# Kernel optimization log

Hardware: AMD Instinct MI355X
Metric: run time of the kernel (lower is better)

Reference implementation:

```python
import jax, jax.numpy as jnp
import numpy as np

B, P, M, C = 64, 8732, 16, 81
THRESHOLD = 0.5
NEG_POS_RATIO = 3
ALPHA = 1.0  # config.reg_weights
EPS = 1e-7


def cxcy_to_xy(c):
    return jnp.concatenate([c[..., :2] - c[..., 2:] / 2.0,
                            c[..., :2] + c[..., 2:] / 2.0], axis=-1)


def _rand_boxes_cxcy(key, shape):
    k1, k2 = jax.random.split(key)
    cxcy = jax.random.uniform(k1, shape + (2,), minval=0.2, maxval=0.8)
    wh = jax.random.uniform(k2, shape + (2,), minval=0.05, maxval=0.35)
    return jnp.concatenate([cxcy, wh], axis=-1)


def setup_inputs() -> dict:
    key = jax.random.key(0)
    ks = jax.random.split(key, 5)
    predicted_locs = cxcy_to_xy(_rand_boxes_cxcy(ks[0], (B, P)))          # valid corner boxes
    predicted_scores = jax.random.normal(ks[1], (B, P, C), dtype=jnp.float32)
    boxes = jnp.clip(cxcy_to_xy(_rand_boxes_cxcy(ks[2], (B, M))), 0.0, 1.0)  # GT corner boxes
    labels = jax.random.randint(ks[3], (B, M), 1, C)                       # object labels (1..C-1)
    priors_cxcy = _rand_boxes_cxcy(ks[4], (P,))
    return {"predicted_locs": predicted_locs, "predicted_scores": predicted_scores,
            "boxes": boxes, "labels": labels, "priors_cxcy": priors_cxcy}


def jaccard(a, b):
    # a: [M,4], b: [P,4] corner boxes -> [M,P] IoU
    lt = jnp.maximum(a[:, None, :2], b[None, :, :2])
    rb = jnp.minimum(a[:, None, 2:], b[None, :, 2:])
    wh = jnp.clip(rb - lt, 0.0)
    inter = wh[..., 0] * wh[..., 1]
    area_a = (a[:, 2] - a[:, 0]) * (a[:, 3] - a[:, 1])
    area_b = (b[:, 2] - b[:, 0]) * (b[:, 3] - b[:, 1])
    return inter / (area_a[:, None] + area_b[None, :] - inter)


def diou_loss(b1, b2):
    # corner boxes, elementwise over leading dims -> per-box loss 1 - DIoU
    lt = jnp.maximum(b1[..., :2], b2[..., :2])
    rb = jnp.minimum(b1[..., 2:], b2[..., 2:])
    wh = jnp.clip(rb - lt, 0.0)
    inter = wh[..., 0] * wh[..., 1]
    area1 = (b1[..., 2] - b1[..., 0]) * (b1[..., 3] - b1[..., 1])
    area2 = (b2[..., 2] - b2[..., 0]) * (b2[..., 3] - b2[..., 1])
    iou = inter / (area1 + area2 - inter + EPS)
    c1 = (b1[..., :2] + b1[..., 2:]) / 2.0
    c2 = (b2[..., :2] + b2[..., 2:]) / 2.0
    inter_diag = jnp.sum((c1 - c2) ** 2, axis=-1)
    enc_lt = jnp.minimum(b1[..., :2], b2[..., :2])
    enc_rb = jnp.maximum(b1[..., 2:], b2[..., 2:])
    outer_diag = jnp.sum((enc_rb - enc_lt) ** 2, axis=-1)
    dious = jnp.clip(iou - inter_diag / (outer_diag + EPS), -1.0, 1.0)
    return 1.0 - dious


def reference(predicted_locs, predicted_scores, boxes, labels, priors_cxcy):
    priors_xy = cxcy_to_xy(priors_cxcy)

    def assign(boxes_i, labels_i):
        overlap = jaccard(boxes_i, priors_xy)              # [M, P]
        ovl_prior = overlap.max(axis=0)                    # best overlap per prior
        obj_prior = overlap.argmax(axis=0)                 # best object per prior
        ovl_obj = overlap.max(axis=1)                      # best overlap per object
        prior_obj = overlap.argmax(axis=1)                 # best prior per object
        valid = ovl_obj > 0
        j_idx = jnp.cumsum(valid.astype(jnp.int32)) - 1    # index within filtered list (faithful)
        idx = jnp.where(valid, prior_obj, P)               # P -> dropped (out of bounds)
        ovl_prior = ovl_prior.at[idx].set(1.0, mode='drop')
        obj_prior = obj_prior.at[idx].set(j_idx, mode='drop')
        lab = labels_i[obj_prior]
        label_pos = jnp.where(ovl_prior < THRESHOLD, 0, lab)
        label_neg = jnp.where(ovl_prior < THRESHOLD - 0.1, -1, lab)
        return label_pos, label_neg

    true_classes, true_neg_classes = jax.vmap(assign)(boxes, labels)  # [B,P] each
    positive = true_classes > 0                                        # [B,P]
    pos_f = positive.astype(jnp.float32)
    n_pos_total = jnp.sum(pos_f)

    # Localization loss: DIoU(pred_pos, pred_pos) with reduce='mean' (faithful to source)
    per_box = diou_loss(predicted_locs, predicted_locs)                # [B,P]
    loc_loss = jnp.sum(per_box * pos_f) / jnp.maximum(n_pos_total, 1.0)

    # Confidence loss: per-prior CE + hard-negative mining (neg_pos_ratio)
    logp = jax.nn.log_softmax(predicted_scores, axis=-1)
    conf_all = -jnp.take_along_axis(logp, true_classes[..., None], axis=-1)[..., 0]  # [B,P]
    conf_pos_sum = jnp.sum(conf_all * pos_f)
    conf_neg = jnp.where(positive, 0.0, conf_all)
    conf_neg_sorted = -jnp.sort(-conf_neg, axis=-1)                    # descending
    n_hard = NEG_POS_RATIO * jnp.sum(positive, axis=1)                 # [B]
    hard_mask = (jnp.arange(P)[None, :] < n_hard[:, None]).astype(jnp.float32)
    conf_loss = (jnp.sum(conf_neg_sorted * hard_mask) + conf_pos_sum) / n_pos_total

    return conf_loss + ALPHA * loc_loss
```

## Files before the change

### kernel.cpp

```cpp
#include <hip/hip_runtime.h>
#include <math.h>

#define B_ 64
#define P_ 8732
#define M_ 16
#define C_ 81
#define THRESH 0.5f
#define EPS_ 1e-7f

#define CE_TILE 64
#define NBLK_CE ((B_ * P_) / CE_TILE)

__global__ __launch_bounds__(1024) void assign_kernel(
    const float* __restrict__ boxes,
    const int*   __restrict__ labels,
    const float* __restrict__ priors,
    int*         __restrict__ true_classes,
    int*         __restrict__ n_pos)
{
    const int b = blockIdx.x;
    const int tid = threadIdx.x;
    const int lane = tid & 63;
    const int wv = tid >> 6;

    __shared__ float s_ovl[P_];
    __shared__ unsigned char s_obj[P_];
    __shared__ float s_bx[M_][4];
    __shared__ float s_barea[M_];
    __shared__ int   s_lab[M_];
    __shared__ float s_wv[M_][16];
    __shared__ int   s_wp[M_][16];
    __shared__ float s_ovl_obj[M_];
    __shared__ int   s_prior_obj[M_];
    __shared__ int   s_cnt[16];

    if (tid < M_*4) ((float*)s_bx)[tid] = boxes[b*M_*4 + tid];
    if (tid < M_)   s_lab[tid] = labels[b*M_ + tid];
    __syncthreads();
    if (tid < M_)
        s_barea[tid] = (s_bx[tid][2]-s_bx[tid][0])*(s_bx[tid][3]-s_bx[tid][1]);
    __syncthreads();

    float bestv[M_]; int bestp[M_];
    #pragma unroll
    for (int m = 0; m < M_; ++m) { bestv[m] = -1.0f; bestp[m] = 0x7fffffff; }

    for (int p = tid; p < P_; p += 1024) {
        float4 pc = ((const float4*)priors)[p];
        float px1 = pc.x - pc.z*0.5f, py1 = pc.y - pc.w*0.5f;
        float px2 = pc.x + pc.z*0.5f, py2 = pc.y + pc.w*0.5f;
        float parea = (px2-px1)*(py2-py1);
        float bv = -1.0f; int bm = 0;
        #pragma unroll
        for (int m = 0; m < M_; ++m) {
            float ix1 = fmaxf(s_bx[m][0], px1);
            float iy1 = fmaxf(s_bx[m][1], py1);
            float ix2 = fminf(s_bx[m][2], px2);
            float iy2 = fminf(s_bx[m][3], py2);
            float iw = fmaxf(ix2-ix1, 0.0f);
            float ih = fmaxf(iy2-iy1, 0.0f);
            float inter = iw*ih;
            float iou = inter / (s_barea[m] + parea - inter);
            if (iou > bv) { bv = iou; bm = m; }
            if (iou > bestv[m]) { bestv[m] = iou; bestp[m] = p; }
        }
        s_ovl[p] = bv;
        s_obj[p] = (unsigned char)bm;
    }

    #pragma unroll
    for (int m = 0; m < M_; ++m) {
        float v = bestv[m]; int p = bestp[m];
        #pragma unroll
        for (int o = 32; o; o >>= 1) {
            float v2 = __shfl_xor(v, o);
            int   p2 = __shfl_xor(p, o);
            if (v2 > v || (v2 == v && p2 < p)) { v = v2; p = p2; }
        }
        if (lane == 0) { s_wv[m][wv] = v; s_wp[m][wv] = p; }
    }
    __syncthreads();

    if (tid < M_) {
        float v = s_wv[tid][0]; int p = s_wp[tid][0];
        #pragma unroll
        for (int w = 1; w < 16; ++w) {
            float v2 = s_wv[tid][w]; int p2 = s_wp[tid][w];
            if (v2 > v || (v2 == v && p2 < p)) { v = v2; p = p2; }
        }
        s_ovl_obj[tid] = v; s_prior_obj[tid] = p;
    }
    __syncthreads();

    if (tid == 0) {
        int cnt = 0;
        for (int m = 0; m < M_; ++m) {
            if (s_ovl_obj[m] > 0.0f) {
                int p = s_prior_obj[m];
                s_ovl[p] = 1.0f;
                s_obj[p] = (unsigned char)cnt;
                cnt++;
            }
        }
    }
    __syncthreads();

    int cpos = 0;
    for (int p = tid; p < P_; p += 1024) {
        int tc = 0;
        if (!(s_ovl[p] < THRESH)) tc = s_lab[s_obj[p]];
        true_classes[(size_t)b*P_ + p] = tc;
        cpos += (tc > 0);
    }
    #pragma unroll
    for (int o = 32; o; o >>= 1) cpos += __shfl_xor(cpos, o);
    if (lane == 0) s_cnt[wv] = cpos;
    __syncthreads();
    if (tid == 0) {
        int t = 0;
        #pragma unroll
        for (int w = 0; w < 16; ++w) t += s_cnt[w];
        n_pos[b] = t;
    }
}

__global__ __launch_bounds__(256) void ce_loc_kernel(
    const float* __restrict__ scores,
    const float* __restrict__ locs,
    const int*   __restrict__ tcls,
    float*       __restrict__ conf_neg,
    float*       __restrict__ blk_pos,
    float*       __restrict__ blk_loc)
{
    __shared__ float s[CE_TILE * C_];
    __shared__ int   s_tc[CE_TILE];
    __shared__ float s_cf[CE_TILE];
    __shared__ float s_red[4][2];

    const int tid  = threadIdx.x;
    const int tile = blockIdx.x;
    const int lane = tid & 63;
    const int wv   = tid >> 6;

    {
        const float4* g4 = (const float4*)(scores + (size_t)tile * CE_TILE * C_);
        float4* s4 = (float4*)s;
        #pragma unroll
        for (int k = 0; k < 5; ++k) s4[tid + 256*k] = g4[tid + 256*k];
        if (tid < 1296 - 1280) s4[tid + 1280] = g4[tid + 1280];
        if (tid < CE_TILE) s_tc[tid] = tcls[tile * CE_TILE + tid];
    }
    __syncthreads();

    const int q    = tid & 3;
    const int lrow = tid >> 2;
    const float* row = s + lrow * C_;

    float x[21];
    #pragma unroll
    for (int k = 0; k < 21; ++k) {
        const int idx = q + 4*k;
        x[k] = (idx < C_) ? row[idx] : -INFINITY;
    }

    float mx = x[0];
    #pragma unroll
    for (int k = 1; k < 21; ++k) mx = fmaxf(mx, x[k]);
    mx = fmaxf(mx, __shfl_xor(mx, 1));
    mx = fmaxf(mx, __shfl_xor(mx, 2));

    float e = 0.f;
    #pragma unroll
    for (int k = 0; k < 21; ++k) e += __expf(x[k] - mx);
    e += __shfl_xor(e, 1);
    e += __shfl_xor(e, 2);

    float p_acc = 0.f, l_acc = 0.f;
    if (q == 0) {
        const int r = tile * CE_TILE + lrow;
        const int t = s_tc[lrow];
        float conf = mx + __logf(e) - row[t];
        if (t > 0) {
            s_cf[lrow] = 0.f;
            p_acc = conf;
            float4 bx = ((const float4*)locs)[r];
            float w = bx.z - bx.x, h = bx.w - bx.y;
            float iw = fmaxf(w, 0.f), ih = fmaxf(h, 0.f);
            float inter = iw * ih;
            float area  = w * h;
            float iou   = inter / (area + area - inter + EPS_);
            float diou  = fminf(fmaxf(iou, -1.f), 1.f);
            l_acc = 1.f - diou;
        } else {
            s_cf[lrow] = fmaxf(conf, 0.f);
        }
    }

    #pragma unroll
    for (int o = 32; o; o >>= 1) {
        p_acc += __shfl_xor(p_acc, o);
        l_acc += __shfl_xor(l_acc, o);
    }
    if (lane == 0) { s_red[wv][0] = p_acc; s_red[wv][1] = l_acc; }
    __syncthreads();

    if (wv == 0) conf_neg[tile * CE_TILE + lane] = s_cf[lane];
    if (tid == 0) {
        blk_pos[tile] = s_red[0][0] + s_red[1][0] + s_red[2][0] + s_red[3][0];
        blk_loc[tile] = s_red[0][1] + s_red[1][1] + s_red[2][1] + s_red[3][1];
    }
}

__global__ __launch_bounds__(1024) void topk_kernel(
    const float* __restrict__ conf_neg,
    const int*   __restrict__ n_pos,
    float*       __restrict__ hard)
{
    const int b = blockIdx.x;
    const int tid = threadIdx.x;
    const int lane = tid & 63;
    const int wv = tid >> 6;

    __shared__ float s_v[P_];
    __shared__ int   s_hist[16][256];
    __shared__ int   s_cg[257];
    __shared__ int   s_sel;
    __shared__ int   s_t[16];
    __shared__ float s_f[16];

    for (int i = tid; i < P_; i += 1024) s_v[i] = conf_neg[(size_t)b*P_ + i];
    int k = 3 * n_pos[b];
    if (k <= 0) { if (tid == 0) hard[b] = 0.f; return; }
    if (k > P_) k = P_;
    __syncthreads();

    const unsigned masks[4]  = {0u, 0xFF800000u, 0xFFFF8000u, 0xFFFFFF80u};
    const int      shifts[4] = {23, 15, 7, 0};

    unsigned prefix = 0u;
    int k_rem = k;

    for (int rd = 0; rd < 4; ++rd) {
        const unsigned hm = masks[rd];
        const int sh = shifts[rd];

        ((int*)s_hist)[tid] = 0;
        ((int*)s_hist)[tid + 1024] = 0;
        ((int*)s_hist)[tid + 2048] = 0;
        ((int*)s_hist)[tid + 3072] = 0;
        __syncthreads();

        for (int i = tid; i < P_; i += 1024) {
            unsigned u = __float_as_uint(s_v[i]);
            if ((u & hm) == prefix)
                atomicAdd(&s_hist[wv][(u >> sh) & 0xFF], 1);
        }
        __syncthreads();

        if (wv == 0) {
            int carry = 0;
            for (int c = 3; c >= 0; --c) {
                int bin = c * 64 + lane;
                int tot = 0;
                #pragma unroll
                for (int w = 0; w < 16; ++w) tot += s_hist[w][bin];
                #pragma unroll
                for (int o = 1; o < 64; o <<= 1) {
                    int v = __shfl_down(tot, o);
                    if (lane + o < 64) tot += v;
                }
                int cg = tot + carry;
                s_cg[bin] = cg;
                carry = __shfl(cg, 0);
            }
            if (lane == 0) s_cg[256] = 0;
        }
        __syncthreads();

        if (tid < 256) {
            if (s_cg[tid] >= k_rem && s_cg[tid + 1] < k_rem) s_sel = tid;
        }
        __syncthreads();

        const int bsel = s_sel;
        k_rem -= s_cg[bsel + 1];
        prefix |= (unsigned)bsel << sh;
        __syncthreads();
    }

    const float tval = __uint_as_float(prefix);

    float sum = 0.f; int cgt = 0;
    for (int i = tid; i < P_; i += 1024) {
        float v = s_v[i];
        if (v > tval) { sum += v; cgt++; }
    }
    #pragma unroll
    for (int o = 32; o; o >>= 1) { sum += __shfl_xor(sum, o); cgt += __shfl_xor(cgt, o); }
    if (lane == 0) { s_f[wv] = sum; s_t[wv] = cgt; }
    __syncthreads();
    if (tid == 0) {
        float s = 0.f; int c = 0;
        #pragma unroll
        for (int w = 0; w < 16; ++w) { s += s_f[w]; c += s_t[w]; }
        hard[b] = s + (float)(k - c) * tval;
    }
}

__global__ __launch_bounds__(256) void final_kernel(
    const float* __restrict__ blk_pos,
    const float* __restrict__ blk_loc,
    const float* __restrict__ hard,
    const int*   __restrict__ n_pos,
    float*       __restrict__ out)
{
    const int tid = threadIdx.x;
    const int lane = tid & 63;
    const int wv = tid >> 6;
    __shared__ double sd[4][4];

    double p = 0.0, l = 0.0, h = 0.0, np = 0.0;
    for (int i = tid; i < NBLK_CE; i += 256) { p += blk_pos[i]; l += blk_loc[i]; }
    if (tid < B_) { h = hard[tid]; np = (double)n_pos[tid]; }

    #pragma unroll
    for (int o = 32; o; o >>= 1) {
        p += __shfl_xor(p, o); l += __shfl_xor(l, o);
        h += __shfl_xor(h, o); np += __shfl_xor(np, o);
    }
    if (lane == 0) { sd[wv][0] = p; sd[wv][1] = l; sd[wv][2] = h; sd[wv][3] = np; }
    __syncthreads();
    if (tid == 0) {
        double tp = 0, tl = 0, th = 0, tn = 0;
        #pragma unroll
        for (int w = 0; w < 4; ++w) { tp += sd[w][0]; tl += sd[w][1]; th += sd[w][2]; tn += sd[w][3]; }
        double conf_loss = (th + tp) / tn;
        double loc_loss  = tl / fmax(tn, 1.0);
        out[0] = (float)(conf_loss + 1.0 * loc_loss);
    }
}

extern "C" void kernel_launch(void* const* d_in, const int* in_sizes, int n_in,
                              void* d_out, int out_size, void* d_ws, size_t ws_size,
                              hipStream_t stream) {
    const float* predicted_locs   = (const float*)d_in[0];
    const float* predicted_scores = (const float*)d_in[1];
    const float* boxes            = (const float*)d_in[2];
    const int*   labels           = (const int*)d_in[3];
    const float* priors           = (const float*)d_in[4];
    float* out = (float*)d_out;

    char* ws = (char*)d_ws;
    size_t off = 0;
    int*    true_classes = (int*)(ws + off);   off += sizeof(int)   * (size_t)B_ * P_;
    float*  conf_neg     = (float*)(ws + off); off += sizeof(float) * (size_t)B_ * P_;
    int*    n_pos        = (int*)(ws + off);   off += sizeof(int)   * B_;
    float*  hard         = (float*)(ws + off); off += sizeof(float) * B_;
    float*  blk_pos      = (float*)(ws + off); off += sizeof(float) * NBLK_CE;
    float*  blk_loc      = (float*)(ws + off); off += sizeof(float) * NBLK_CE;

    assign_kernel<<<B_, 1024, 0, stream>>>(boxes, labels, priors,
                                           true_classes, n_pos);
    ce_loc_kernel<<<NBLK_CE, 256, 0, stream>>>(predicted_scores, predicted_locs,
                                               true_classes, conf_neg,
                                               blk_pos, blk_loc);
    topk_kernel<<<B_, 1024, 0, stream>>>(conf_neg, n_pos, hard);
    final_kernel<<<1, 256, 0, stream>>>(blk_pos, blk_loc, hard, n_pos, out);
}
```

Baseline: 360.8 us.

## Fuse top-k and final reduction into CE kernel via last-block-done counters

Merges the CE/loc, top-k radix select and final reduction kernels into one launch. Each CE block atomically adds its row count to a per-batch counter, and whichever block completes a batch runs the radix select for that batch from global memory with 256 threads. A global done counter then elects the last block to compute the final loss. This removes two kernel launches and the device-wide gap before top-k starts, but serializes each batch's top-k onto a single 256-thread block reading from L2 instead of a 1024-thread block working from LDS.

```diff
diff --git a/kernel.cpp b/kernel.cpp
--- a/kernel.cpp
+++ b/kernel.cpp
@@ -16,7 +16,9 @@
     const int*   __restrict__ labels,
     const float* __restrict__ priors,
     int*         __restrict__ true_classes,
-    int*         __restrict__ n_pos)
+    int*         __restrict__ n_pos,
+    int*         __restrict__ cnt,
+    int*         __restrict__ done)
 {
     const int b = blockIdx.x;
     const int tid = threadIdx.x;
@@ -33,6 +35,11 @@
     __shared__ float s_ovl_obj[M_];
     __shared__ int   s_prior_obj[M_];
     __shared__ int   s_cnt[16];
+
+    if (tid == 0) {
+        atomicExch(&cnt[b], 0);
+        if (b == 0) atomicExch(done, 0);
+    }
 
     if (tid < M_*4) ((float*)s_bx)[tid] = boxes[b*M_*4 + tid];
     if (tid < M_)   s_lab[tid] = labels[b*M_ + tid];
@@ -93,13 +100,13 @@
     __syncthreads();
 
     if (tid == 0) {
-        int cnt = 0;
+        int c = 0;
         for (int m = 0; m < M_; ++m) {
             if (s_ovl_obj[m] > 0.0f) {
                 int p = s_prior_obj[m];
                 s_ovl[p] = 1.0f;
-                s_obj[p] = (unsigned char)cnt;
-                cnt++;
+                s_obj[p] = (unsigned char)c;
+                c++;
             }
         }
     }
@@ -124,37 +131,146 @@
     }
 }
 
-__global__ __launch_bounds__(256) void ce_loc_kernel(
+struct SA { float s[CE_TILE*C_]; int tc[CE_TILE]; float cf[CE_TILE]; float red[4][2]; };
+struct SB { int hist[4][256]; int cg[257]; float f[4]; int t[4]; int sel; };
+union SMem { SA a; SB b; };
+
+__device__ void do_topk(int bx, const float* __restrict__ conf_neg,
+                        const int* __restrict__ n_pos,
+                        const float* __restrict__ blk_pos,
+                        const float* __restrict__ blk_loc,
+                        float* __restrict__ hard,
+                        float* __restrict__ partial_p,
+                        float* __restrict__ partial_l,
+                        SMem& sm, int tid, int lane, int wv)
+{
+    {
+        const int s0 = (bx * P_ + CE_TILE - 1) / CE_TILE;
+        const int s1 = ((bx + 1) * P_ + CE_TILE - 1) / CE_TILE;
+        float sp = 0.f, sl = 0.f;
+        for (int t = s0 + tid; t < s1; t += 256) { sp += blk_pos[t]; sl += blk_loc[t]; }
+        #pragma unroll
+        for (int o = 32; o; o >>= 1) { sp += __shfl_xor(sp, o); sl += __shfl_xor(sl, o); }
+        if (lane == 0) { sm.b.f[wv] = sp; sm.b.cg[wv] = __float_as_int(sl); }
+        __syncthreads();
+        if (tid == 0) {
+            partial_p[bx] = sm.b.f[0] + sm.b.f[1] + sm.b.f[2] + sm.b.f[3];
+            partial_l[bx] = __int_as_float(sm.b.cg[0]) + __int_as_float(sm.b.cg[1])
+                          + __int_as_float(sm.b.cg[2]) + __int_as_float(sm.b.cg[3]);
+        }
+        __syncthreads();
+    }
+
+    int k = 3 * n_pos[bx];
+    if (k <= 0) { if (tid == 0) hard[bx] = 0.f; return; }
+    if (k > P_) k = P_;
+
+    const float* cv = conf_neg + (size_t)bx * P_;
+    const unsigned masks[4]  = {0u, 0xFF800000u, 0xFFFF8000u, 0xFFFFFF80u};
+    const int      shifts[4] = {23, 15, 7, 0};
+    unsigned prefix = 0u;
+    int k_rem = k;
+
+    for (int rd = 0; rd < 4; ++rd) {
+        const unsigned hm = masks[rd];
+        const int sh = shifts[rd];
+
+        #pragma unroll
+        for (int i = 0; i < 4; ++i) ((int*)sm.b.hist)[tid + 256*i] = 0;
+        __syncthreads();
+
+        for (int i = tid; i < P_; i += 256) {
+            unsigned u = __float_as_uint(cv[i]);
+            if ((u & hm) == prefix)
+                atomicAdd(&sm.b.hist[wv][(u >> sh) & 0xFF], 1);
+        }
+        __syncthreads();
+
+        if (tid < 64) {
+            int carry = 0;
+            for (int c = 3; c >= 0; --c) {
+                int bin = c * 64 + lane;
+                int tot = sm.b.hist[0][bin] + sm.b.hist[1][bin]
+                        + sm.b.hist[2][bin] + sm.b.hist[3][bin];
+                #pragma unroll
+                for (int o = 1; o < 64; o <<= 1) {
+                    int v = __shfl_down(tot, o);
+                    if (lane + o < 64) tot += v;
+                }
+                int cg = tot + carry;
+                sm.b.cg[bin] = cg;
+                carry = __shfl(cg, 0);
+            }
+            if (lane == 0) sm.b.cg[256] = 0;
+        }
+        __syncthreads();
+
+        if (sm.b.cg[tid] >= k_rem && sm.b.cg[tid + 1] < k_rem) sm.b.sel = tid;
+        __syncthreads();
+
+        const int bsel = sm.b.sel;
+        k_rem -= sm.b.cg[bsel + 1];
+        prefix |= (unsigned)bsel << sh;
+        __syncthreads();
+    }
+
+    const float tval = __uint_as_float(prefix);
+    float sum = 0.f; int cgt = 0;
+    for (int i = tid; i < P_; i += 256) {
+        float v = cv[i];
+        if (v > tval) { sum += v; cgt++; }
+    }
+    #pragma unroll
+    for (int o = 32; o; o >>= 1) { sum += __shfl_xor(sum, o); cgt += __shfl_xor(cgt, o); }
+    if (lane == 0) { sm.b.f[wv] = sum; sm.b.t[wv] = cgt; }
+    __syncthreads();
+    if (tid == 0) {
+        float s = sm.b.f[0] + sm.b.f[1] + sm.b.f[2] + sm.b.f[3];
+        int   c = sm.b.t[0] + sm.b.t[1] + sm.b.t[2] + sm.b.t[3];
+        hard[bx] = s + (float)(k - c) * tval;
+    }
+    __syncthreads();
+}
+
+__global__ __launch_bounds__(256) void fused_kernel(
     const float* __restrict__ scores,
     const float* __restrict__ locs,
     const int*   __restrict__ tcls,
+    const int*   __restrict__ n_pos,
     float*       __restrict__ conf_neg,
     float*       __restrict__ blk_pos,
-    float*       __restrict__ blk_loc)
+    float*       __restrict__ blk_loc,
+    float*       __restrict__ hard,
+    float*       __restrict__ partial_p,
+    float*       __restrict__ partial_l,
+    int*         __restrict__ cnt,
+    int*         __restrict__ done,
+    float*       __restrict__ out)
 {
-    __shared__ float s[CE_TILE * C_];
-    __shared__ int   s_tc[CE_TILE];
-    __shared__ float s_cf[CE_TILE];
-    __shared__ float s_red[4][2];
+    __shared__ SMem sm;
+    __shared__ int s_todo[2];
+    __shared__ int s_final;
 
     const int tid  = threadIdx.x;
     const int tile = blockIdx.x;
     const int lane = tid & 63;
     const int wv   = tid >> 6;
 
+    if (tid == 0) { s_todo[0] = -1; s_todo[1] = -1; s_final = 0; }
+
     {
         const float4* g4 = (const float4*)(scores + (size_t)tile * CE_TILE * C_);
-        float4* s4 = (float4*)s;
+        float4* s4 = (float4*)sm.a.s;
         #pragma unroll
         for (int k = 0; k < 5; ++k) s4[tid + 256*k] = g4[tid + 256*k];
-        if (tid < 1296 - 1280) s4[tid + 1280] = g4[tid + 1280];
-        if (tid < CE_TILE) s_tc[tid] = tcls[tile * CE_TILE + tid];
+        if (tid < 16) s4[tid + 1280] = g4[tid + 1280];
+        if (tid < CE_TILE) sm.a.tc[tid] = tcls[tile * CE_TILE + tid];
     }
     __syncthreads();
 
     const int q    = tid & 3;
     const int lrow = tid >> 2;
-    const float* row = s + lrow * C_;
+    const float* row = sm.a.s + lrow * C_;
 
     float x[21];
     #pragma unroll
@@ -162,13 +278,11 @@
         const int idx = q + 4*k;
         x[k] = (idx < C_) ? row[idx] : -INFINITY;
     }
-
     float mx = x[0];
     #pragma unroll
     for (int k = 1; k < 21; ++k) mx = fmaxf(mx, x[k]);
     mx = fmaxf(mx, __shfl_xor(mx, 1));
     mx = fmaxf(mx, __shfl_xor(mx, 2));
-
     float e = 0.f;
     #pragma unroll
     for (int k = 0; k < 21; ++k) e += __expf(x[k] - mx);
@@ -178,10 +292,10 @@
     float p_acc = 0.f, l_acc = 0.f;
     if (q == 0) {
         const int r = tile * CE_TILE + lrow;
-        const int t = s_tc[lrow];
+        const int t = sm.a.tc[lrow];
         float conf = mx + __logf(e) - row[t];
         if (t > 0) {
-            s_cf[lrow] = 0.f;
+            sm.a.cf[lrow] = 0.f;
             p_acc = conf;
             float4 bx = ((const float4*)locs)[r];
             float w = bx.z - bx.x, h = bx.w - bx.y;
@@ -192,151 +306,74 @@
             float diou  = fminf(fmaxf(iou, -1.f), 1.f);
             l_acc = 1.f - diou;
         } else {
-            s_cf[lrow] = fmaxf(conf, 0.f);
-        }
-    }
-
+            sm.a.cf[lrow] = fmaxf(conf, 0.f);
+        }
+    }
     #pragma unroll
     for (int o = 32; o; o >>= 1) {
         p_acc += __shfl_xor(p_acc, o);
         l_acc += __shfl_xor(l_acc, o);
     }
-    if (lane == 0) { s_red[wv][0] = p_acc; s_red[wv][1] = l_acc; }
-    __syncthreads();
-
-    if (wv == 0) conf_neg[tile * CE_TILE + lane] = s_cf[lane];
-    if (tid == 0) {
-        blk_pos[tile] = s_red[0][0] + s_red[1][0] + s_red[2][0] + s_red[3][0];
-        blk_loc[tile] = s_red[0][1] + s_red[1][1] + s_red[2][1] + s_red[3][1];
-    }
-}
-
-__global__ __launch_bounds__(1024) void topk_kernel(
-    const float* __restrict__ conf_neg,
-    const int*   __restrict__ n_pos,
-    float*       __restrict__ hard)
-{
-    const int b = blockIdx.x;
-    const int tid = threadIdx.x;
-    const int lane = tid & 63;
-    const int wv = tid >> 6;
-
-    __shared__ float s_v[P_];
-    __shared__ int   s_hist[16][256];
-    __shared__ int   s_cg[257];
-    __shared__ int   s_sel;
-    __shared__ int   s_t[16];
-    __shared__ float s_f[16];
-
-    for (int i = tid; i < P_; i += 1024) s_v[i] = conf_neg[(size_t)b*P_ + i];
-    int k = 3 * n_pos[b];
-    if (k <= 0) { if (tid == 0) hard[b] = 0.f; return; }
-    if (k > P_) k = P_;
-    __syncthreads();
-
-    const unsigned masks[4]  = {0u, 0xFF800000u, 0xFFFF8000u, 0xFFFFFF80u};
-    const int      shifts[4] = {23, 15, 7, 0};
-
-    unsigned prefix = 0u;
-    int k_rem = k;
-
-    for (int rd = 0; rd < 4; ++rd) {
-        const unsigned hm = masks[rd];
-        const int sh = shifts[rd];
-
-        ((int*)s_hist)[tid] = 0;
-        ((int*)s_hist)[tid + 1024] = 0;
-        ((int*)s_hist)[tid + 2048] = 0;
-        ((int*)s_hist)[tid + 3072] = 0;
-        __syncthreads();
-
-        for (int i = tid; i < P_; i += 1024) {
-            unsigned u = __float_as_uint(s_v[i]);
-            if ((u & hm) == prefix)
-                atomicAdd(&s_hist[wv][(u >> sh) & 0xFF], 1);
-        }
-        __syncthreads();
-
-        if (wv == 0) {
-            int carry = 0;
-            for (int c = 3; c >= 0; --c) {
-                int bin = c * 64 + lane;
-                int tot = 0;
-                #pragma unroll
-                for (int w = 0; w < 16; ++w) tot += s_hist[w][bin];
-                #pragma unroll
-                for (int o = 1; o < 64; o <<= 1) {
-                    int v = __shfl_down(tot, o);
-                    if (lane + o < 64) tot += v;
-                }
-                int cg = tot + carry;
-                s_cg[bin] = cg;
-                carry = __shfl(cg, 0);
+    if (lane == 0) { sm.a.red[wv][0] = p_acc; sm.a.red[wv][1] = l_acc; }
+    __syncthreads();
+
+    if (wv == 0) conf_neg[tile * CE_TILE + lane] = sm.a.cf[lane];
+    if (tid == 0) {
+        blk_pos[tile] = sm.a.red[0][0] + sm.a.red[1][0] + sm.a.red[2][0] + sm.a.red[3][0];
+        blk_loc[tile] = sm.a.red[0][1] + sm.a.red[1][1] + sm.a.red[2][1] + sm.a.red[3][1];
+    }
+    __syncthreads();
+
+    if (tid == 0) {
+        const int r0 = tile * CE_TILE;
+        const int b0 = r0 / P_;
+        const int end0 = (b0 + 1) * P_;
+        const int n0 = min(CE_TILE, end0 - r0);
+        const int n1 = CE_TILE - n0;
+        __threadfence();
+        int nw = 0;
+        if (atomicAdd(&cnt[b0], n0) + n0 == P_) s_todo[nw++] = b0;
+        if (n1 > 0) {
+            if (atomicAdd(&cnt[b0 + 1], n1) + n1 == P_) s_todo[nw++] = b0 + 1;
+        }
+        if (nw) __threadfence();
+    }
+    __syncthreads();
+
+    int ncomp = 0;
+    #pragma unroll
+    for (int i = 0; i < 2; ++i) {
+        const int bx = s_todo[i];
+        if (bx >= 0) {
+            do_topk(bx, conf_neg, n_pos, blk_pos, blk_loc,
+                    hard, partial_p, partial_l, sm, tid, lane, wv);
+            ncomp++;
+        }
+    }
+
+    if (ncomp) {
+        if (tid == 0) {
+            __threadfence();
+            if (atomicAdd(done, ncomp) + ncomp == B_) {
+                __threadfence();
+                s_final = 1;
             }
-            if (lane == 0) s_cg[256] = 0;
-        }
-        __syncthreads();
-
-        if (tid < 256) {
-            if (s_cg[tid] >= k_rem && s_cg[tid + 1] < k_rem) s_sel = tid;
-        }
-        __syncthreads();
-
-        const int bsel = s_sel;
-        k_rem -= s_cg[bsel + 1];
-        prefix |= (unsigned)bsel << sh;
-        __syncthreads();
-    }
-
-    const float tval = __uint_as_float(prefix);
-
-    float sum = 0.f; int cgt = 0;
-    for (int i = tid; i < P_; i += 1024) {
-        float v = s_v[i];
-        if (v > tval) { sum += v; cgt++; }
-    }
-    #pragma unroll
-    for (int o = 32; o; o >>= 1) { sum += __shfl_xor(sum, o); cgt += __shfl_xor(cgt, o); }
-    if (lane == 0) { s_f[wv] = sum; s_t[wv] = cgt; }
-    __syncthreads();
-    if (tid == 0) {
-        float s = 0.f; int c = 0;
-        #pragma unroll
-        for (int w = 0; w < 16; ++w) { s += s_f[w]; c += s_t[w]; }
-        hard[b] = s + (float)(k - c) * tval;
-    }
-}
-
-__global__ __launch_bounds__(256) void final_kernel(
-    const float* __restrict__ blk_pos,
-    const float* __restrict__ blk_loc,
-    const float* __restrict__ hard,
-    const int*   __restrict__ n_pos,
-    float*       __restrict__ out)
-{
-    const int tid = threadIdx.x;
-    const int lane = tid & 63;
-    const int wv = tid >> 6;
-    __shared__ double sd[4][4];
-
-    double p = 0.0, l = 0.0, h = 0.0, np = 0.0;
-    for (int i = tid; i < NBLK_CE; i += 256) { p += blk_pos[i]; l += blk_loc[i]; }
-    if (tid < B_) { h = hard[tid]; np = (double)n_pos[tid]; }
-
-    #pragma unroll
-    for (int o = 32; o; o >>= 1) {
-        p += __shfl_xor(p, o); l += __shfl_xor(l, o);
-        h += __shfl_xor(h, o); np += __shfl_xor(np, o);
-    }
-    if (lane == 0) { sd[wv][0] = p; sd[wv][1] = l; sd[wv][2] = h; sd[wv][3] = np; }
-    __syncthreads();
-    if (tid == 0) {
-        double tp = 0, tl = 0, th = 0, tn = 0;
-        #pragma unroll
-        for (int w = 0; w < 4; ++w) { tp += sd[w][0]; tl += sd[w][1]; th += sd[w][2]; tn += sd[w][3]; }
-        double conf_loss = (th + tp) / tn;
-        double loc_loss  = tl / fmax(tn, 1.0);
-        out[0] = (float)(conf_loss + 1.0 * loc_loss);
+        }
+        __syncthreads();
+        if (s_final && tid < 64) {
+            double h = hard[tid], pp = partial_p[tid], pl = partial_l[tid];
+            double np = (double)n_pos[tid];
+            #pragma unroll
+            for (int o = 32; o; o >>= 1) {
+                h  += __shfl_xor(h, o);  pp += __shfl_xor(pp, o);
+                pl += __shfl_xor(pl, o); np += __shfl_xor(np, o);
+            }
+            if (tid == 0) {
+                double conf_loss = (h + pp) / np;
+                double loc_loss  = pl / fmax(np, 1.0);
+                out[0] = (float)(conf_loss + loc_loss);
+            }
+        }
     }
 }
 
@@ -354,16 +391,19 @@
     size_t off = 0;
     int*    true_classes = (int*)(ws + off);   off += sizeof(int)   * (size_t)B_ * P_;
     float*  conf_neg     = (float*)(ws + off); off += sizeof(float) * (size_t)B_ * P_;
+    float*  blk_pos      = (float*)(ws + off); off += sizeof(float) * NBLK_CE;
+    float*  blk_loc      = (float*)(ws + off); off += sizeof(float) * NBLK_CE;
     int*    n_pos        = (int*)(ws + off);   off += sizeof(int)   * B_;
     float*  hard         = (float*)(ws + off); off += sizeof(float) * B_;
-    float*  blk_pos      = (float*)(ws + off); off += sizeof(float) * NBLK_CE;
-    float*  blk_loc      = (float*)(ws + off); off += sizeof(float) * NBLK_CE;
+    float*  partial_p    = (float*)(ws + off); off += sizeof(float) * B_;
+    float*  partial_l    = (float*)(ws + off); off += sizeof(float) * B_;
+    int*    cnt          = (int*)(ws + off);   off += sizeof(int)   * B_;
+    int*    done         = (int*)(ws + off);   off += sizeof(int)   * 1;
 
     assign_kernel<<<B_, 1024, 0, stream>>>(boxes, labels, priors,
-                                           true_classes, n_pos);
-    ce_loc_kernel<<<NBLK_CE, 256, 0, stream>>>(predicted_scores, predicted_locs,
-                                               true_classes, conf_neg,
-                                               blk_pos, blk_loc);
-    topk_kernel<<<B_, 1024, 0, stream>>>(conf_neg, n_pos, hard);
-    final_kernel<<<1, 256, 0, stream>>>(blk_pos, blk_loc, hard, n_pos, out);
+                                           true_classes, n_pos, cnt, done);
+    fused_kernel<<<NBLK_CE, 256, 0, stream>>>(predicted_scores, predicted_locs,
+                                              true_classes, n_pos, conf_neg,
+                                              blk_pos, blk_loc, hard,
+                                              partial_p, partial_l, cnt, done, out);
 }
```

New measurement: 744.8 us. 2.06x slower.
